# Optimization experiments

Hardware: AMD Instinct MI355X
Metric: run time of the kernel (lower is better)

The kernel has to match this reference:

```python
import jax, jax.numpy as jnp
import numpy as np

DIM = 64
N = 10000
E = 40000


def setup_inputs() -> dict:
    key = jax.random.key(0)
    ks = jax.random.split(key, 16)
    def rn(k, shape, s):
        return jax.random.normal(k, shape, dtype=jnp.float32) * s
    inp = {}
    inp["x"] = jax.random.normal(ks[0], (N, 3), dtype=jnp.float32)
    inp["edge_attr"] = jax.random.uniform(ks[1], (E, 7), dtype=jnp.float32)
    inp["edge_index"] = jax.random.randint(ks[2], (2, E), 0, N)
    inp["batch"] = jnp.zeros((N,), dtype=jnp.int32)
    # lin0: Linear(3, dim)
    inp["lin0_w"] = rn(ks[3], (DIM, 3), 0.3)
    inp["lin0_b"] = jnp.zeros((DIM,), jnp.float32)
    # edge MLP: Linear(7, dim) -> ReLU -> Linear(dim, dim*dim)
    inp["em1_w"] = rn(ks[4], (DIM, 7), 0.3)
    inp["em1_b"] = jnp.zeros((DIM,), jnp.float32)
    inp["em2_w"] = rn(ks[5], (DIM * DIM, DIM), 0.05)
    inp["em2_b"] = jnp.zeros((DIM * DIM,), jnp.float32)
    # NNConv root weight [in, out] and bias
    inp["root_w"] = rn(ks[6], (DIM, DIM), 0.1)
    inp["conv_b"] = jnp.zeros((DIM,), jnp.float32)
    # GRU(dim, dim), gate order r, z, n
    inp["gru_wih"] = rn(ks[7], (3 * DIM, DIM), 0.1)
    inp["gru_whh"] = rn(ks[8], (3 * DIM, DIM), 0.1)
    inp["gru_bih"] = jnp.zeros((3 * DIM,), jnp.float32)
    inp["gru_bhh"] = jnp.zeros((3 * DIM,), jnp.float32)
    # Set2Set LSTM(2*dim, dim), gate order i, f, g, o
    inp["lstm_wih"] = rn(ks[9], (4 * DIM, 2 * DIM), 0.1)
    inp["lstm_whh"] = rn(ks[10], (4 * DIM, DIM), 0.1)
    inp["lstm_bih"] = jnp.zeros((4 * DIM,), jnp.float32)
    inp["lstm_bhh"] = jnp.zeros((4 * DIM,), jnp.float32)
    inp["lin1_w"] = rn(ks[11], (DIM, 2 * DIM), 0.1)
    inp["lin1_b"] = jnp.zeros((DIM,), jnp.float32)
    inp["lin3_w"] = rn(ks[12], (1, DIM), 0.1)
    inp["lin3_b"] = jnp.zeros((1,), jnp.float32)
    return inp


def _forward(x, edge_attr, lin0_w, lin0_b, em1_w, em1_b, em2_w, em2_b,
             root_w, conv_b, gru_wih, gru_whh, gru_bih, gru_bhh,
             lstm_wih, lstm_whh, lstm_bih, lstm_bhh,
             lin1_w, lin1_b, lin3_w, lin3_b, edge_index, batch):
    n = x.shape[0]
    dim = lin0_w.shape[0]
    src, dst = edge_index[0], edge_index[1]

    out = jax.nn.relu(x @ lin0_w.T + lin0_b)  # [N, dim]
    h = out                                   # GRU hidden state

    # Edge-conditioned weights depend only on edge_attr -> compute once.
    we = jax.nn.relu(edge_attr @ em1_w.T + em1_b) @ em2_w.T + em2_b
    we = we.reshape(-1, dim, dim)             # [E, dim, dim]

    deg = jax.ops.segment_sum(jnp.ones_like(src, dtype=x.dtype), dst, num_segments=n)
    inv_deg = jnp.where(deg > 0, 1.0 / jnp.maximum(deg, 1.0), 0.0)[:, None]

    for _ in range(6):
        # NNConv: per-edge matmul, scatter-mean, plus root transform
        msg = jnp.einsum('ei,eio->eo', out[src], we)            # [E, dim]
        agg = jax.ops.segment_sum(msg, dst, num_segments=n) * inv_deg
        m = jax.nn.relu(out @ root_w + agg + conv_b)            # [N, dim]
        # single-step GRU over nodes (seq_len=1, batch=N)
        gi = m @ gru_wih.T + gru_bih
        gh = h @ gru_whh.T + gru_bhh
        ir, iz, inew = jnp.split(gi, 3, axis=-1)
        hr, hz, hnew = jnp.split(gh, 3, axis=-1)
        r = jax.nn.sigmoid(ir + hr)
        z = jax.nn.sigmoid(iz + hz)
        ncand = jnp.tanh(inew + r * hnew)
        h = (1.0 - z) * ncand + z * h
        out = h

    # Set2Set pooling; single graph (batch is all zeros, pool.view(1,-1))
    q_star = jnp.zeros((1, 2 * dim), x.dtype)
    hl = jnp.zeros((1, dim), x.dtype)
    cl = jnp.zeros((1, dim), x.dtype)
    for _ in range(6):
        g = q_star @ lstm_wih.T + lstm_bih + hl @ lstm_whh.T + lstm_bhh
        gi_, gf_, gg_, go_ = jnp.split(g, 4, axis=-1)
        cl = jax.nn.sigmoid(gf_) * cl + jax.nn.sigmoid(gi_) * jnp.tanh(gg_)
        hl = jax.nn.sigmoid(go_) * jnp.tanh(cl)
        q = hl                                                  # [1, dim]
        e = jnp.einsum('nd,d->n', out, q[0])                    # attention logits
        a = jax.nn.softmax(e)                                   # softmax over the single graph
        r = jnp.einsum('n,nd->d', a, out)[None, :]              # readout [1, dim]
        q_star = jnp.concatenate([q, r], axis=-1)               # [1, 2*dim]

    pool = q_star.reshape(1, -1)
    hid = jax.nn.relu(pool @ lin1_w.T + lin1_b)
    return hid @ lin3_w.T + lin3_b                              # [1, 1]


def reference(x, edge_attr, edge_index, batch, lin0_w, lin0_b, em1_w, em1_b,
              em2_w, em2_b, root_w, conv_b, gru_wih, gru_whh, gru_bih, gru_bhh,
              lstm_wih, lstm_whh, lstm_bih, lstm_bhh, lin1_w, lin1_b, lin3_w, lin3_b):
    return _forward(x, edge_attr, lin0_w, lin0_b, em1_w, em1_b, em2_w, em2_b,
                    root_w, conv_b, gru_wih, gru_whh, gru_bih, gru_bhh,
                    lstm_wih, lstm_whh, lstm_bih, lstm_bhh,
                    lin1_w, lin1_b, lin3_w, lin3_b, edge_index, batch)
```

## Files before the change

### kernel.cpp

```cpp
#include <hip/hip_runtime.h>
#include <math.h>

#define NNODES 10000
#define NEDGES 40000
#define DIM 64
#define MC 4160
#define WS 200
#define AST2 72

typedef short bf16x8 __attribute__((ext_vector_type(8)));
typedef float floatx4 __attribute__((ext_vector_type(4)));

__device__ __forceinline__ float sigmoidf_(float x) { return 1.0f / (1.0f + expf(-x)); }

__device__ __forceinline__ unsigned short f2bf(float x) {
    unsigned int u = __float_as_uint(x);
    u += 0x7fffu + ((u >> 16) & 1u);
    return (unsigned short)(u >> 16);
}
__device__ __forceinline__ float bf2f(unsigned short h) {
    return __uint_as_float(((unsigned int)h) << 16);
}
__device__ __forceinline__ void write_split(unsigned short* __restrict__ p, int d, float v) {
    unsigned short hi = f2bf(v);
    unsigned short lo = f2bf(v - bf2f(hi));
    p[d] = hi;
    p[64 + d] = hi;
    p[128 + d] = lo;
}

__global__ __launch_bounds__(256) void k_node_init(const float* __restrict__ x,
                                                   const float* __restrict__ w,
                                                   const float* __restrict__ b,
                                                   float* __restrict__ out,
                                                   unsigned short* __restrict__ Abf) {
    int idx = blockIdx.x * 256 + threadIdx.x;
    if (idx >= NNODES * 64) return;
    int n = idx >> 6, d = idx & 63;
    float a = b[d];
    a += x[n * 3 + 0] * w[d * 3 + 0];
    a += x[n * 3 + 1] * w[d * 3 + 1];
    a += x[n * 3 + 2] * w[d * 3 + 2];
    float v = fmaxf(a, 0.0f);
    out[idx] = v;
    write_split(Abf + (size_t)n * 192, d, v);
}

__global__ __launch_bounds__(256) void k_h1(const float* __restrict__ ea,
                                            const float* __restrict__ w,
                                            const float* __restrict__ b,
                                            const int* __restrict__ sortpos,
                                            float* __restrict__ h1s) {
    int idx = blockIdx.x * 256 + threadIdx.x;
    if (idx >= NEDGES * 64) return;
    int e = idx >> 6, d = idx & 63;
    float a = b[d];
#pragma unroll
    for (int j = 0; j < 7; ++j) a += ea[e * 7 + j] * w[d * 7 + j];
    h1s[(size_t)sortpos[e] * 64 + d] = fmaxf(a, 0.0f);
}

__global__ __launch_bounds__(256) void k_w2bt(const float* __restrict__ em2_w,
                                              const float* __restrict__ em2_b,
                                              unsigned short* __restrict__ Bbf) {
    int idx = blockIdx.x * 256 + threadIdx.x;
    if (idx >= 64 * MC) return;
    int c = idx >> 6, i = idx & 63;
    float v;
    if (c < 4096) {
        v = em2_w[((size_t)(i * 64 + (c >> 6))) * 64 + (c & 63)];
    } else {
        v = em2_b[i * 64 + (c - 4096)];
    }
    unsigned short hi = f2bf(v);
    unsigned short lo = f2bf(v - bf2f(hi));
    unsigned short* row = Bbf + (size_t)c * 192;
    row[i] = hi;
    row[64 + i] = lo;
    row[128 + i] = hi;
}

__global__ __launch_bounds__(256) void k_wb(const float* __restrict__ root_w,
                                            const float* __restrict__ wih,
                                            const float* __restrict__ whh,
                                            unsigned short* __restrict__ Wcat) {
    int idx = blockIdx.x * 256 + threadIdx.x;
    if (idx >= 448 * 64) return;
    int r = idx >> 6, i = idx & 63;
    float v;
    if (r < 64) v = root_w[i * 64 + r];
    else if (r < 256) v = wih[(r - 64) * 64 + i];
    else v = whh[(r - 256) * 64 + i];
    unsigned short hi = f2bf(v);
    unsigned short lo = f2bf(v - bf2f(hi));
    unsigned short* row = Wcat + (size_t)r * 192;
    row[i] = hi;
    row[64 + i] = lo;
    row[128 + i] = hi;
}

__global__ __launch_bounds__(256) void k_lstmT2(const float* __restrict__ wih,
                                                const float* __restrict__ whh,
                                                float* __restrict__ wcT,
                                                float* __restrict__ wrT) {
    int idx = blockIdx.x * 256 + threadIdx.x;
    if (idx < 64 * 256) {
        int k = idx >> 8, t = idx & 255;
        wcT[idx] = wih[t * 128 + k] + whh[t * 64 + k];
    } else if (idx < 2 * 64 * 256) {
        int i2 = idx - 64 * 256;
        int k = i2 >> 8, t = i2 & 255;
        wrT[i2] = wih[t * 128 + 64 + k];
    }
}

__global__ __launch_bounds__(256) void k_hist(const int* __restrict__ ei,
                                              int* __restrict__ counts,
                                              float* __restrict__ deg) {
    int e = blockIdx.x * 256 + threadIdx.x;
    if (e < NEDGES) {
        atomicAdd(&counts[ei[e]], 1);
        atomicAdd(&deg[ei[NEDGES + e]], 1.0f);
    }
}

__global__ __launch_bounds__(256) void k_scan(const int* __restrict__ counts,
                                              int* __restrict__ row_start,
                                              int* __restrict__ cursor) {
    __shared__ int partial[256];
    const int tid = threadIdx.x;
    const int base = tid * 40;
    int local[40];
    int sum = 0;
#pragma unroll
    for (int i = 0; i < 40; ++i) {
        int idx = base + i;
        int v = (idx < NNODES) ? counts[idx] : 0;
        local[i] = sum;
        sum += v;
    }
    partial[tid] = sum;
    __syncthreads();
    for (int off = 1; off < 256; off <<= 1) {
        int t = (tid >= off) ? partial[tid - off] : 0;
        __syncthreads();
        partial[tid] += t;
        __syncthreads();
    }
    const int prev = (tid > 0) ? partial[tid - 1] : 0;
#pragma unroll
    for (int i = 0; i < 40; ++i) {
        int idx = base + i;
        if (idx < NNODES) {
            int rs = prev + local[i];
            row_start[idx] = rs;
            cursor[idx] = rs;
        }
    }
    if (tid == 255) row_start[NNODES] = partial[255];
}

__global__ __launch_bounds__(256) void k_scatter(const int* __restrict__ ei,
                                                 int* __restrict__ cursor,
                                                 int* __restrict__ sortpos,
                                                 int* __restrict__ dst_s) {
    int e = blockIdx.x * 256 + threadIdx.x;
    if (e < NEDGES) {
        int s = ei[e];
        int pos = atomicAdd(&cursor[s], 1);
        sortpos[e] = pos;
        dst_s[pos] = ei[NEDGES + e];
    }
}

__global__ __launch_bounds__(256) void k_invdeg(const float* __restrict__ deg, float* __restrict__ inv) {
    int n = blockIdx.x * 256 + threadIdx.x;
    if (n < NNODES) {
        float dg = deg[n];
        inv[n] = dg > 0.0f ? 1.0f / dg : 0.0f;
    }
}

__global__ __launch_bounds__(256) void k_gemmM(const unsigned short* __restrict__ Abf,
                                               const unsigned short* __restrict__ Bbf,
                                               unsigned short* __restrict__ Mb) {
    __shared__ __align__(16) unsigned short As[64 * AST2];
    __shared__ __align__(16) unsigned short Bs[64 * AST2];
    __shared__ __align__(16) float Cs[64 * 68];
    const int tid = threadIdx.x;
    const int col0 = blockIdx.x * 64;
    const int wave = tid >> 6, lane = tid & 63;
    const int mi = lane & 15, q = lane >> 4;
#pragma unroll
    for (int j = 0; j < 2; ++j) {
        int idx = tid + 256 * j;
        int r = idx >> 3, c8 = (idx & 7) * 8;
        *reinterpret_cast<uint4*>(&Bs[r * AST2 + c8]) =
            *reinterpret_cast<const uint4*>(&Bbf[(size_t)(col0 + r) * 192 + c8]);
    }
    for (int rt = 0; rt < 4; ++rt) {
        const int row0 = (blockIdx.y * 4 + rt) * 64;
#pragma unroll
        for (int j = 0; j < 2; ++j) {
            int idx = tid + 256 * j;
            int r = idx >> 3, c8 = (idx & 7) * 8;
            int ra = row0 + r;
            if (ra >= NNODES) ra = NNODES - 1;
            *reinterpret_cast<uint4*>(&As[r * AST2 + c8]) =
                *reinterpret_cast<const uint4*>(&Abf[(size_t)ra * 192 + c8]);
        }
        __syncthreads();
        floatx4 acc[4];
#pragma unroll
        for (int nt = 0; nt < 4; ++nt)
#pragma unroll
            for (int r = 0; r < 4; ++r) acc[nt][r] = 0.0f;
        const unsigned short* arow = &As[(wave * 16 + mi) * AST2 + q * 8];
#pragma unroll
        for (int ks = 0; ks < 2; ++ks) {
            bf16x8 a = *reinterpret_cast<const bf16x8*>(arow + ks * 32);
#pragma unroll
            for (int nt = 0; nt < 4; ++nt) {
                bf16x8 b = *reinterpret_cast<const bf16x8*>(&Bs[(nt * 16 + mi) * AST2 + ks * 32 + q * 8]);
                acc[nt] = __builtin_amdgcn_mfma_f32_16x16x32_bf16(a, b, acc[nt], 0, 0, 0);
            }
        }
        const int rl = wave * 16 + q * 4;
#pragma unroll
        for (int nt = 0; nt < 4; ++nt)
#pragma unroll
            for (int r = 0; r < 4; ++r)
                Cs[(rl + r) * 68 + nt * 16 + mi] = acc[nt][r];
        __syncthreads();
#pragma unroll
        for (int j = 0; j < 2; ++j) {
            int idx = tid + 256 * j;
            int r = idx >> 3, c8 = (idx & 7) * 8;
            int row = row0 + r;
            if (row < NNODES) {
                const float* src = &Cs[r * 68 + c8];
                unsigned int p0 = (unsigned int)f2bf(src[0]) | ((unsigned int)f2bf(src[1]) << 16);
                unsigned int p1 = (unsigned int)f2bf(src[2]) | ((unsigned int)f2bf(src[3]) << 16);
                unsigned int p2 = (unsigned int)f2bf(src[4]) | ((unsigned int)f2bf(src[5]) << 16);
                unsigned int p3 = (unsigned int)f2bf(src[6]) | ((unsigned int)f2bf(src[7]) << 16);
                *reinterpret_cast<uint4*>(&Mb[(size_t)row * MC + col0 + c8]) =
                    make_uint4(p0, p1, p2, p3);
            }
        }
        __syncthreads();
    }
}

__global__ __launch_bounds__(256) void k_msg(const unsigned short* __restrict__ Mb,
                                             const float* __restrict__ h1s,
                                             const int* __restrict__ row_start,
                                             const int* __restrict__ dst_s,
                                             float* __restrict__ agg) {
    const int w = threadIdx.x >> 6;
    const int o = threadIdx.x & 63;
    const int s = blockIdx.x * 4 + w;
    const int e0 = row_start[s], e1 = row_start[s + 1];
    if (e0 == e1) return;
    const unsigned short* mrow = Mb + (size_t)s * MC + o * 64;
    uint4 m[8];
#pragma unroll
    for (int j = 0; j < 8; ++j)
        m[j] = *reinterpret_cast<const uint4*>(mrow + j * 8);
    const float bias = bf2f(Mb[(size_t)s * MC + 4096 + o]);
    for (int e = e0; e < e1; ++e) {
        const float4* hv = reinterpret_cast<const float4*>(h1s + (size_t)e * 64);
        float acc = bias;
#pragma unroll
        for (int j = 0; j < 8; ++j) {
            float4 ha = hv[2 * j];
            float4 hb = hv[2 * j + 1];
            unsigned int u;
            u = m[j].x;
            acc += ha.x * __uint_as_float(u << 16) + ha.y * __uint_as_float(u & 0xffff0000u);
            u = m[j].y;
            acc += ha.z * __uint_as_float(u << 16) + ha.w * __uint_as_float(u & 0xffff0000u);
            u = m[j].z;
            acc += hb.x * __uint_as_float(u << 16) + hb.y * __uint_as_float(u & 0xffff0000u);
            u = m[j].w;
            acc += hb.z * __uint_as_float(u << 16) + hb.w * __uint_as_float(u & 0xffff0000u);
        }
        atomicAdd(&agg[(size_t)dst_s[e] * 64 + o], acc);
    }
}

__global__ __launch_bounds__(256) void k_node(float* __restrict__ agg,
                                              const float* __restrict__ invdeg,
                                              const unsigned short* __restrict__ Wcat,
                                              const float* __restrict__ conv_b,
                                              const float* __restrict__ bih,
                                              const float* __restrict__ bhh,
                                              float* __restrict__ out,
                                              unsigned short* __restrict__ Abf) {
    __shared__ unsigned short As[64 * WS];
    __shared__ unsigned short Ms[64 * WS];
    __shared__ unsigned short Bs[192 * WS];
    __shared__ float ho[64 * 68];
    const int tid = threadIdx.x;
    const int row0 = blockIdx.x * 64;
#pragma unroll
    for (int j = 0; j < 6; ++j) {
        int idx = tid + 256 * j;
        int r = idx / 24, jj = idx % 24;
        int ra = row0 + r; if (ra >= NNODES) ra = NNODES - 1;
        *reinterpret_cast<uint4*>(&As[r * WS + jj * 8]) =
            *reinterpret_cast<const uint4*>(&Abf[(size_t)ra * 192 + jj * 8]);
    }
#pragma unroll
    for (int j = 0; j < 4; ++j) {
        int idx = tid + 256 * j;
        int r = idx >> 4, c4 = (idx & 15) * 4;
        int ra = row0 + r; if (ra >= NNODES) ra = NNODES - 1;
        *reinterpret_cast<float4*>(&ho[r * 68 + c4]) =
            *reinterpret_cast<const float4*>(&out[(size_t)ra * 64 + c4]);
    }
#pragma unroll
    for (int j = 0; j < 18; ++j) {
        int idx = tid + 256 * j;
        int r = idx / 24, jj = idx % 24;
        *reinterpret_cast<uint4*>(&Bs[r * WS + jj * 8]) =
            *reinterpret_cast<const uint4*>(&Wcat[(size_t)(256 + r) * 192 + jj * 8]);
    }
    __syncthreads();
    const int wave = tid >> 6, lane = tid & 63;
    const int mi = lane & 15, q = lane >> 4;
    const int d = wave * 16 + mi;
    floatx4 gh[4][3];
#pragma unroll
    for (int rt = 0; rt < 4; ++rt)
#pragma unroll
        for (int g = 0; g < 3; ++g)
#pragma unroll
            for (int r = 0; r < 4; ++r) gh[rt][g][r] = 0.0f;
#pragma unroll
    for (int ks = 0; ks < 6; ++ks) {
        bf16x8 b[3];
#pragma unroll
        for (int g = 0; g < 3; ++g)
            b[g] = *reinterpret_cast<const bf16x8*>(&Bs[(g * 64 + d) * WS + ks * 32 + q * 8]);
#pragma unroll
        for (int rt = 0; rt < 4; ++rt) {
            bf16x8 a = *reinterpret_cast<const bf16x8*>(&As[(rt * 16 + mi) * WS + ks * 32 + q * 8]);
#pragma unroll
            for (int g = 0; g < 3; ++g)
                gh[rt][g] = __builtin_amdgcn_mfma_f32_16x16x32_bf16(a, b[g], gh[rt][g], 0, 0, 0);
        }
    }
    __syncthreads();
#pragma unroll
    for (int j = 0; j < 6; ++j) {
        int idx = tid + 256 * j;
        int r = idx / 24, jj = idx % 24;
        *reinterpret_cast<uint4*>(&Bs[r * WS + jj * 8]) =
            *reinterpret_cast<const uint4*>(&Wcat[(size_t)r * 192 + jj * 8]);
    }
    __syncthreads();
    {
        floatx4 cm[4];
#pragma unroll
        for (int rt = 0; rt < 4; ++rt)
#pragma unroll
            for (int r = 0; r < 4; ++r) cm[rt][r] = 0.0f;
#pragma unroll
        for (int ks = 0; ks < 6; ++ks) {
            bf16x8 b = *reinterpret_cast<const bf16x8*>(&Bs[d * WS + ks * 32 + q * 8]);
#pragma unroll
            for (int rt = 0; rt < 4; ++rt) {
                bf16x8 a = *reinterpret_cast<const bf16x8*>(&As[(rt * 16 + mi) * WS + ks * 32 + q * 8]);
                cm[rt] = __builtin_amdgcn_mfma_f32_16x16x32_bf16(a, b, cm[rt], 0, 0, 0);
            }
        }
        const float cb = conv_b[d];
#pragma unroll
        for (int rt = 0; rt < 4; ++rt) {
#pragma unroll
            for (int r = 0; r < 4; ++r) {
                int row = rt * 16 + q * 4 + r;
                int ra = row0 + row; int rc = (ra < NNODES) ? ra : NNODES - 1;
                float v = cm[rt][r] + agg[(size_t)rc * 64 + d] * invdeg[rc] + cb;
                if (ra < NNODES) agg[(size_t)ra * 64 + d] = 0.0f;
                v = fmaxf(v, 0.0f);
                unsigned short hi = f2bf(v);
                unsigned short lo = f2bf(v - bf2f(hi));
                Ms[row * WS + d] = hi;
                Ms[row * WS + 64 + d] = hi;
                Ms[row * WS + 128 + d] = lo;
            }
        }
    }
    __syncthreads();
#pragma unroll
    for (int j = 0; j < 18; ++j) {
        int idx = tid + 256 * j;
        int r = idx / 24, jj = idx % 24;
        *reinterpret_cast<uint4*>(&Bs[r * WS + jj * 8]) =
            *reinterpret_cast<const uint4*>(&Wcat[(size_t)(64 + r) * 192 + jj * 8]);
    }
    __syncthreads();
    floatx4 gi[4][3];
#pragma unroll
    for (int rt = 0; rt < 4; ++rt)
#pragma unroll
        for (int g = 0; g < 3; ++g)
#pragma unroll
            for (int r = 0; r < 4; ++r) gi[rt][g][r] = 0.0f;
#pragma unroll
    for (int ks = 0; ks < 6; ++ks) {
        bf16x8 b[3];
#pragma unroll
        for (int g = 0; g < 3; ++g)
            b[g] = *reinterpret_cast<const bf16x8*>(&Bs[(g * 64 + d) * WS + ks * 32 + q * 8]);
#pragma unroll
        for (int rt = 0; rt < 4; ++rt) {
            bf16x8 a = *reinterpret_cast<const bf16x8*>(&Ms[(rt * 16 + mi) * WS + ks * 32 + q * 8]);
#pragma unroll
            for (int g = 0; g < 3; ++g)
                gi[rt][g] = __builtin_amdgcn_mfma_f32_16x16x32_bf16(a, b[g], gi[rt][g], 0, 0, 0);
        }
    }
    const float bi_r = bih[d], bi_z = bih[64 + d], bi_n = bih[128 + d];
    const float bh_r = bhh[d], bh_z = bhh[64 + d], bh_n = bhh[128 + d];
#pragma unroll
    for (int rt = 0; rt < 4; ++rt) {
#pragma unroll
        for (int r = 0; r < 4; ++r) {
            int row = rt * 16 + q * 4 + r;
            int ra = row0 + row;
            float rr = sigmoidf_(gi[rt][0][r] + bi_r + gh[rt][0][r] + bh_r);
            float zz = sigmoidf_(gi[rt][1][r] + bi_z + gh[rt][1][r] + bh_z);
            float nc = tanhf(gi[rt][2][r] + bi_n + rr * (gh[rt][2][r] + bh_n));
            float hn = (1.0f - zz) * nc + zz * ho[row * 68 + d];
            if (ra < NNODES) {
                out[(size_t)ra * 64 + d] = hn;
                write_split(Abf + (size_t)ra * 192, d, hn);
            }
        }
    }
}

__global__ __launch_bounds__(256) void k_step(const float* __restrict__ out,
                                              const float* __restrict__ wcT,
                                              const float* __restrict__ wrT,
                                              const float* __restrict__ bih,
                                              const float* __restrict__ bhh,
                                              float* __restrict__ hc,
                                              float* rs,
                                              int it) {
    __shared__ float outs[256 * 65];
    __shared__ float hl_s[64];
    __shared__ float qr[64];
    __shared__ float gsh[256];
    __shared__ float wsh[256];
    __shared__ float red[256];
    const int tid = threadIdx.x;
    const int n0 = blockIdx.x * 256;
#pragma unroll
    for (int j = 0; j < 16; ++j) {
        int idx = tid + 256 * j;
        int r = idx >> 4, c4 = (idx & 15) * 4;
        int n = n0 + r;
        float4 v = make_float4(0.0f, 0.0f, 0.0f, 0.0f);
        if (n < NNODES) v = *reinterpret_cast<const float4*>(&out[(size_t)n * 64 + c4]);
        outs[r * 65 + c4 + 0] = v.x;
        outs[r * 65 + c4 + 1] = v.y;
        outs[r * 65 + c4 + 2] = v.z;
        outs[r * 65 + c4 + 3] = v.w;
    }
    if (tid < 64) {
        hl_s[tid] = hc[it * 128 + tid];
        qr[tid] = (it > 0) ? rs[it * 68 + tid] / rs[it * 68 + 64] : 0.0f;
    }
    __syncthreads();
    float g0 = 0.0f, g1 = 0.0f, g2 = 0.0f, g3 = 0.0f;
#pragma unroll 4
    for (int k = 0; k < 64; k += 4) {
        g0 += hl_s[k + 0] * wcT[(k + 0) * 256 + tid] + qr[k + 0] * wrT[(k + 0) * 256 + tid];
        g1 += hl_s[k + 1] * wcT[(k + 1) * 256 + tid] + qr[k + 1] * wrT[(k + 1) * 256 + tid];
        g2 += hl_s[k + 2] * wcT[(k + 2) * 256 + tid] + qr[k + 2] * wrT[(k + 2) * 256 + tid];
        g3 += hl_s[k + 3] * wcT[(k + 3) * 256 + tid] + qr[k + 3] * wrT[(k + 3) * 256 + tid];
    }
    gsh[tid] = bih[tid] + bhh[tid] + ((g0 + g1) + (g2 + g3));
    __syncthreads();
    if (tid < 64) {
        float ig = sigmoidf_(gsh[tid]);
        float fg = sigmoidf_(gsh[64 + tid]);
        float gg = tanhf(gsh[128 + tid]);
        float og = sigmoidf_(gsh[192 + tid]);
        float c = fg * hc[it * 128 + 64 + tid] + ig * gg;
        float h = og * tanhf(c);
        hl_s[tid] = h;
        hc[(it + 1) * 128 + tid] = h;
        hc[(it + 1) * 128 + 64 + tid] = c;
    }
    __syncthreads();
    float w = 0.0f;
    if (n0 + tid < NNODES) {
        const float* row = &outs[tid * 65];
        float e0 = 0.0f, e1 = 0.0f, e2 = 0.0f, e3 = 0.0f;
#pragma unroll 8
        for (int k = 0; k < 64; k += 4) {
            e0 += row[k + 0] * hl_s[k + 0];
            e1 += row[k + 1] * hl_s[k + 1];
            e2 += row[k + 2] * hl_s[k + 2];
            e3 += row[k + 3] * hl_s[k + 3];
        }
        w = expf((e0 + e1) + (e2 + e3));
    }
    wsh[tid] = w;
    red[tid] = w;
    __syncthreads();
    for (int s = 128; s > 0; s >>= 1) {
        if (tid < s) red[tid] += red[tid + s];
        __syncthreads();
    }
    if (tid == 0) atomicAdd(&rs[(it + 1) * 68 + 64], red[0]);
    const int grp = tid >> 6, d = tid & 63;
    float a0 = 0.0f, a1 = 0.0f;
#pragma unroll 8
    for (int j = 0; j < 64; j += 2) {
        a0 += wsh[grp * 64 + j] * outs[(grp * 64 + j) * 65 + d];
        a1 += wsh[grp * 64 + j + 1] * outs[(grp * 64 + j + 1) * 65 + d];
    }
    atomicAdd(&rs[(it + 1) * 68 + d], a0 + a1);
}

__global__ __launch_bounds__(128) void k_out(const float* __restrict__ hc,
                                             const float* __restrict__ rs,
                                             const float* __restrict__ lin1_w,
                                             const float* __restrict__ lin1_b,
                                             const float* __restrict__ lin3_w,
                                             const float* __restrict__ lin3_b,
                                             float* __restrict__ dout) {
    __shared__ float qs[128];
    __shared__ float hs[64];
    int tid = threadIdx.x;
    qs[tid] = (tid < 64) ? hc[6 * 128 + tid] : rs[6 * 68 + (tid - 64)] / rs[6 * 68 + 64];
    __syncthreads();
    if (tid < 64) {
        float a = lin1_b[tid];
        for (int k = 0; k < 128; ++k) a += qs[k] * lin1_w[tid * 128 + k];
        hs[tid] = fmaxf(a, 0.0f);
    }
    __syncthreads();
    if (tid == 0) {
        float a = lin3_b[0];
        for (int k = 0; k < 64; ++k) a += hs[k] * lin3_w[k];
        dout[0] = a;
    }
}

extern "C" void kernel_launch(void* const* d_in, const int* in_sizes, int n_in,
                              void* d_out, int out_size, void* d_ws, size_t ws_size,
                              hipStream_t stream) {
    const float* x         = (const float*)d_in[0];
    const float* edge_attr = (const float*)d_in[1];
    const int*   ei        = (const int*)d_in[2];
    const float* lin0_w    = (const float*)d_in[4];
    const float* lin0_b    = (const float*)d_in[5];
    const float* em1_w     = (const float*)d_in[6];
    const float* em1_b     = (const float*)d_in[7];
    const float* em2_w     = (const float*)d_in[8];
    const float* em2_b     = (const float*)d_in[9];
    const float* root_w    = (const float*)d_in[10];
    const float* conv_b    = (const float*)d_in[11];
    const float* gru_wih   = (const float*)d_in[12];
    const float* gru_whh   = (const float*)d_in[13];
    const float* gru_bih   = (const float*)d_in[14];
    const float* gru_bhh   = (const float*)d_in[15];
    const float* lstm_wih  = (const float*)d_in[16];
    const float* lstm_whh  = (const float*)d_in[17];
    const float* lstm_bih  = (const float*)d_in[18];
    const float* lstm_bhh  = (const float*)d_in[19];
    const float* lin1_w    = (const float*)d_in[20];
    const float* lin1_b    = (const float*)d_in[21];
    const float* lin3_w    = (const float*)d_in[22];
    const float* lin3_b    = (const float*)d_in[23];

    float* ws = (float*)d_ws;
    size_t off = 0;
    unsigned short* Mb   = (unsigned short*)(ws + off); off += (size_t)NNODES * MC / 2;
    unsigned short* Abf  = (unsigned short*)(ws + off); off += (size_t)NNODES * 192 / 2;
    unsigned short* Bbf  = (unsigned short*)(ws + off); off += (size_t)MC * 192 / 2;
    unsigned short* Wcat = (unsigned short*)(ws + off); off += (size_t)448 * 192 / 2;
    float* h1s   = ws + off; off += (size_t)NEDGES * 64;
    float* outb  = ws + off; off += (size_t)NNODES * 64;
    float* agg   = ws + off; off += (size_t)NNODES * 64;
    float* deg   = ws + off; off += NNODES;
    int*   counts    = (int*)(ws + off); off += NNODES;
    int*   cursor    = (int*)(ws + off); off += NNODES;
    int*   row_start = (int*)(ws + off); off += NNODES + 4;
    int*   sortpos   = (int*)(ws + off); off += NEDGES;
    int*   dst_s     = (int*)(ws + off); off += NEDGES;
    float* invd  = ws + off; off += NNODES;
    float* wcT   = ws + off; off += 64 * 256;
    float* wrT   = ws + off; off += 64 * 256;
    float* rs    = ws + off; off += 7 * 68;
    float* hc    = ws + off; off += 7 * 128;

    k_node_init<<<2500, 256, 0, stream>>>(x, lin0_w, lin0_b, outb, Abf);
    k_w2bt<<<(64 * MC + 255) / 256, 256, 0, stream>>>(em2_w, em2_b, Bbf);
    k_wb<<<(448 * 64 + 255) / 256, 256, 0, stream>>>(root_w, gru_wih, gru_whh, Wcat);
    k_lstmT2<<<128, 256, 0, stream>>>(lstm_wih, lstm_whh, wcT, wrT);
    hipMemsetAsync(deg, 0, 3 * NNODES * sizeof(float), stream);
    hipMemsetAsync(agg, 0, (size_t)NNODES * 64 * sizeof(float), stream);
    hipMemsetAsync(rs, 0, (7 * 68 + 7 * 128) * sizeof(float), stream);
    k_hist<<<(NEDGES + 255) / 256, 256, 0, stream>>>(ei, counts, deg);
    k_scan<<<1, 256, 0, stream>>>(counts, row_start, cursor);
    k_scatter<<<(NEDGES + 255) / 256, 256, 0, stream>>>(ei, cursor, sortpos, dst_s);
    k_invdeg<<<(NNODES + 255) / 256, 256, 0, stream>>>(deg, invd);
    k_h1<<<10000, 256, 0, stream>>>(edge_attr, em1_w, em1_b, sortpos, h1s);

    for (int t = 0; t < 6; ++t) {
        k_gemmM<<<dim3(65, 40), 256, 0, stream>>>(Abf, Bbf, Mb);
        k_msg<<<2500, 256, 0, stream>>>(Mb, h1s, row_start, dst_s, agg);
        k_node<<<157, 256, 0, stream>>>(agg, invd, Wcat, conv_b, gru_bih, gru_bhh,
                                        outb, Abf);
    }

    for (int it = 0; it < 6; ++it)
        k_step<<<40, 256, 0, stream>>>(outb, wcT, wrT, lstm_bih, lstm_bhh, hc, rs, it);
    k_out<<<1, 128, 0, stream>>>(hc, rs, lin1_w, lin1_b, lin3_w, lin3_b, (float*)d_out);
}
```

Before: 687.8 us.

## Fuse per-node message-weight GEMM with edge message aggregation via LDS

Merges the GEMM that produced the per-node bf16 message matrix (10000 x 4160) with the edge message kernel. Each 512-thread block computes the matrices for 14 source nodes into shared memory and immediately uses them to process those nodes' outgoing edges. This removes the large global write and re-read of the intermediate matrix in every iteration. In exchange it uses about 131 KB of LDS per block, which limits occupancy, and B fragments are read straight from global memory by each block without LDS staging.

New measurement: 810.9 us. 1.18x slower.

```diff
diff --git a/kernel.cpp b/kernel.cpp
--- a/kernel.cpp
+++ b/kernel.cpp
@@ -4,9 +4,10 @@
 #define NNODES 10000
 #define NEDGES 40000
 #define DIM 64
-#define MC 4160
 #define WS 200
-#define AST2 72
+#define MROWS 14
+#define MGS 72
+#define MRS 4680
 
 typedef short bf16x8 __attribute__((ext_vector_type(8)));
 typedef float floatx4 __attribute__((ext_vector_type(4)));
@@ -64,7 +65,7 @@
                                               const float* __restrict__ em2_b,
                                               unsigned short* __restrict__ Bbf) {
     int idx = blockIdx.x * 256 + threadIdx.x;
-    if (idx >= 64 * MC) return;
+    if (idx >= 64 * 4160) return;
     int c = idx >> 6, i = idx & 63;
     float v;
     if (c < 4096) {
@@ -181,110 +182,111 @@
     }
 }
 
-__global__ __launch_bounds__(256) void k_gemmM(const unsigned short* __restrict__ Abf,
+__global__ __launch_bounds__(512) void k_fused(const unsigned short* __restrict__ Abf,
                                                const unsigned short* __restrict__ Bbf,
-                                               unsigned short* __restrict__ Mb) {
-    __shared__ __align__(16) unsigned short As[64 * AST2];
-    __shared__ __align__(16) unsigned short Bs[64 * AST2];
-    __shared__ __align__(16) float Cs[64 * 68];
+                                               const float* __restrict__ h1s,
+                                               const int* __restrict__ row_start,
+                                               const int* __restrict__ dst_s,
+                                               float* __restrict__ agg) {
+    __shared__ __align__(16) unsigned short Mush[MROWS * MRS];
     const int tid = threadIdx.x;
-    const int col0 = blockIdx.x * 64;
-    const int wave = tid >> 6, lane = tid & 63;
+    const int w = tid >> 6, lane = tid & 63;
     const int mi = lane & 15, q = lane >> 4;
-#pragma unroll
-    for (int j = 0; j < 2; ++j) {
-        int idx = tid + 256 * j;
-        int r = idx >> 3, c8 = (idx & 7) * 8;
-        *reinterpret_cast<uint4*>(&Bs[r * AST2 + c8]) =
-            *reinterpret_cast<const uint4*>(&Bbf[(size_t)(col0 + r) * 192 + c8]);
-    }
-    for (int rt = 0; rt < 4; ++rt) {
-        const int row0 = (blockIdx.y * 4 + rt) * 64;
-#pragma unroll
-        for (int j = 0; j < 2; ++j) {
-            int idx = tid + 256 * j;
-            int r = idx >> 3, c8 = (idx & 7) * 8;
-            int ra = row0 + r;
-            if (ra >= NNODES) ra = NNODES - 1;
-            *reinterpret_cast<uint4*>(&As[r * AST2 + c8]) =
-                *reinterpret_cast<const uint4*>(&Abf[(size_t)ra * 192 + c8]);
-        }
-        __syncthreads();
-        floatx4 acc[4];
-#pragma unroll
-        for (int nt = 0; nt < 4; ++nt)
-#pragma unroll
-            for (int r = 0; r < 4; ++r) acc[nt][r] = 0.0f;
-        const unsigned short* arow = &As[(wave * 16 + mi) * AST2 + q * 8];
-#pragma unroll
-        for (int ks = 0; ks < 2; ++ks) {
-            bf16x8 a = *reinterpret_cast<const bf16x8*>(arow + ks * 32);
+    const int s0 = blockIdx.x * MROWS;
+    int ar = s0 + mi; if (ar >= NNODES) ar = NNODES - 1;
+    const bf16x8 a0 = *reinterpret_cast<const bf16x8*>(&Abf[(size_t)ar * 192 + q * 8]);
+    const bf16x8 a1 = *reinterpret_cast<const bf16x8*>(&Abf[(size_t)ar * 192 + 32 + q * 8]);
+    for (int c = w; c < 65; c += 16) {
+        const int c2 = c + 8;
+        bf16x8 bA[8], bB[8];
+#pragma unroll
+        for (int nt = 0; nt < 4; ++nt) {
+            const size_t rb = (size_t)(c * 64 + nt * 16 + mi) * 192;
+            bA[nt]     = *reinterpret_cast<const bf16x8*>(&Bbf[rb + q * 8]);
+            bA[4 + nt] = *reinterpret_cast<const bf16x8*>(&Bbf[rb + 32 + q * 8]);
+        }
+        if (c2 < 65) {
 #pragma unroll
             for (int nt = 0; nt < 4; ++nt) {
-                bf16x8 b = *reinterpret_cast<const bf16x8*>(&Bs[(nt * 16 + mi) * AST2 + ks * 32 + q * 8]);
-                acc[nt] = __builtin_amdgcn_mfma_f32_16x16x32_bf16(a, b, acc[nt], 0, 0, 0);
+                const size_t rb = (size_t)(c2 * 64 + nt * 16 + mi) * 192;
+                bB[nt]     = *reinterpret_cast<const bf16x8*>(&Bbf[rb + q * 8]);
+                bB[4 + nt] = *reinterpret_cast<const bf16x8*>(&Bbf[rb + 32 + q * 8]);
             }
         }
-        const int rl = wave * 16 + q * 4;
-#pragma unroll
-        for (int nt = 0; nt < 4; ++nt)
-#pragma unroll
-            for (int r = 0; r < 4; ++r)
-                Cs[(rl + r) * 68 + nt * 16 + mi] = acc[nt][r];
-        __syncthreads();
-#pragma unroll
-        for (int j = 0; j < 2; ++j) {
-            int idx = tid + 256 * j;
-            int r = idx >> 3, c8 = (idx & 7) * 8;
-            int row = row0 + r;
-            if (row < NNODES) {
-                const float* src = &Cs[r * 68 + c8];
-                unsigned int p0 = (unsigned int)f2bf(src[0]) | ((unsigned int)f2bf(src[1]) << 16);
-                unsigned int p1 = (unsigned int)f2bf(src[2]) | ((unsigned int)f2bf(src[3]) << 16);
-                unsigned int p2 = (unsigned int)f2bf(src[4]) | ((unsigned int)f2bf(src[5]) << 16);
-                unsigned int p3 = (unsigned int)f2bf(src[6]) | ((unsigned int)f2bf(src[7]) << 16);
-                *reinterpret_cast<uint4*>(&Mb[(size_t)row * MC + col0 + c8]) =
-                    make_uint4(p0, p1, p2, p3);
+        {
+            floatx4 acc[4];
+#pragma unroll
+            for (int nt = 0; nt < 4; ++nt)
+#pragma unroll
+                for (int r = 0; r < 4; ++r) acc[nt][r] = 0.0f;
+#pragma unroll
+            for (int nt = 0; nt < 4; ++nt) {
+                acc[nt] = __builtin_amdgcn_mfma_f32_16x16x32_bf16(a0, bA[nt], acc[nt], 0, 0, 0);
+                acc[nt] = __builtin_amdgcn_mfma_f32_16x16x32_bf16(a1, bA[4 + nt], acc[nt], 0, 0, 0);
             }
-        }
-        __syncthreads();
-    }
-}
-
-__global__ __launch_bounds__(256) void k_msg(const unsigned short* __restrict__ Mb,
-                                             const float* __restrict__ h1s,
-                                             const int* __restrict__ row_start,
-                                             const int* __restrict__ dst_s,
-                                             float* __restrict__ agg) {
-    const int w = threadIdx.x >> 6;
-    const int o = threadIdx.x & 63;
-    const int s = blockIdx.x * 4 + w;
-    const int e0 = row_start[s], e1 = row_start[s + 1];
-    if (e0 == e1) return;
-    const unsigned short* mrow = Mb + (size_t)s * MC + o * 64;
-    uint4 m[8];
-#pragma unroll
-    for (int j = 0; j < 8; ++j)
-        m[j] = *reinterpret_cast<const uint4*>(mrow + j * 8);
-    const float bias = bf2f(Mb[(size_t)s * MC + 4096 + o]);
-    for (int e = e0; e < e1; ++e) {
-        const float4* hv = reinterpret_cast<const float4*>(h1s + (size_t)e * 64);
-        float acc = bias;
-#pragma unroll
-        for (int j = 0; j < 8; ++j) {
-            float4 ha = hv[2 * j];
-            float4 hb = hv[2 * j + 1];
-            unsigned int u;
-            u = m[j].x;
-            acc += ha.x * __uint_as_float(u << 16) + ha.y * __uint_as_float(u & 0xffff0000u);
-            u = m[j].y;
-            acc += ha.z * __uint_as_float(u << 16) + ha.w * __uint_as_float(u & 0xffff0000u);
-            u = m[j].z;
-            acc += hb.x * __uint_as_float(u << 16) + hb.y * __uint_as_float(u & 0xffff0000u);
-            u = m[j].w;
-            acc += hb.z * __uint_as_float(u << 16) + hb.w * __uint_as_float(u & 0xffff0000u);
-        }
-        atomicAdd(&agg[(size_t)dst_s[e] * 64 + o], acc);
+#pragma unroll
+            for (int nt = 0; nt < 4; ++nt)
+#pragma unroll
+                for (int r = 0; r < 4; ++r) {
+                    int rr = q * 4 + r;
+                    if (rr < MROWS)
+                        Mush[rr * MRS + c * MGS + nt * 16 + mi] = f2bf(acc[nt][r]);
+                }
+        }
+        if (c2 < 65) {
+            floatx4 acc[4];
+#pragma unroll
+            for (int nt = 0; nt < 4; ++nt)
+#pragma unroll
+                for (int r = 0; r < 4; ++r) acc[nt][r] = 0.0f;
+#pragma unroll
+            for (int nt = 0; nt < 4; ++nt) {
+                acc[nt] = __builtin_amdgcn_mfma_f32_16x16x32_bf16(a0, bB[nt], acc[nt], 0, 0, 0);
+                acc[nt] = __builtin_amdgcn_mfma_f32_16x16x32_bf16(a1, bB[4 + nt], acc[nt], 0, 0, 0);
+            }
+#pragma unroll
+            for (int nt = 0; nt < 4; ++nt)
+#pragma unroll
+                for (int r = 0; r < 4; ++r) {
+                    int rr = q * 4 + r;
+                    if (rr < MROWS)
+                        Mush[rr * MRS + c2 * MGS + nt * 16 + mi] = f2bf(acc[nt][r]);
+                }
+        }
+    }
+    __syncthreads();
+#pragma unroll
+    for (int t = 0; t < 2; ++t) {
+        const int sl = w * 2 + t;
+        if (sl >= MROWS) continue;
+        const int s = s0 + sl;
+        if (s >= NNODES) continue;
+        const int e0 = row_start[s], e1 = row_start[s + 1];
+        if (e0 == e1) continue;
+        uint4 m[8];
+#pragma unroll
+        for (int j = 0; j < 8; ++j)
+            m[j] = *reinterpret_cast<const uint4*>(&Mush[sl * MRS + lane * MGS + j * 8]);
+        const float bias = bf2f(Mush[sl * MRS + 64 * MGS + lane]);
+        for (int e = e0; e < e1; ++e) {
+            const float4* hv = reinterpret_cast<const float4*>(h1s + (size_t)e * 64);
+            float acc = bias;
+#pragma unroll
+            for (int j = 0; j < 8; ++j) {
+                float4 ha = hv[2 * j];
+                float4 hb = hv[2 * j + 1];
+                unsigned int u;
+                u = m[j].x;
+                acc += ha.x * __uint_as_float(u << 16) + ha.y * __uint_as_float(u & 0xffff0000u);
+                u = m[j].y;
+                acc += ha.z * __uint_as_float(u << 16) + ha.w * __uint_as_float(u & 0xffff0000u);
+                u = m[j].z;
+                acc += hb.x * __uint_as_float(u << 16) + hb.y * __uint_as_float(u & 0xffff0000u);
+                u = m[j].w;
+                acc += hb.z * __uint_as_float(u << 16) + hb.w * __uint_as_float(u & 0xffff0000u);
+            }
+            atomicAdd(&agg[(size_t)dst_s[e] * 64 + lane], acc);
+        }
     }
 }
 
@@ -582,9 +584,8 @@
 
     float* ws = (float*)d_ws;
     size_t off = 0;
-    unsigned short* Mb   = (unsigned short*)(ws + off); off += (size_t)NNODES * MC / 2;
     unsigned short* Abf  = (unsigned short*)(ws + off); off += (size_t)NNODES * 192 / 2;
-    unsigned short* Bbf  = (unsigned short*)(ws + off); off += (size_t)MC * 192 / 2;
+    unsigned short* Bbf  = (unsigned short*)(ws + off); off += (size_t)4160 * 192 / 2;
     unsigned short* Wcat = (unsigned short*)(ws + off); off += (size_t)448 * 192 / 2;
     float* h1s   = ws + off; off += (size_t)NEDGES * 64;
     float* outb  = ws + off; off += (size_t)NNODES * 64;
@@ -602,7 +603,7 @@
     float* hc    = ws + off; off += 7 * 128;
 
     k_node_init<<<2500, 256, 0, stream>>>(x, lin0_w, lin0_b, outb, Abf);
-    k_w2bt<<<(64 * MC + 255) / 256, 256, 0, stream>>>(em2_w, em2_b, Bbf);
+    k_w2bt<<<(64 * 4160 + 255) / 256, 256, 0, stream>>>(em2_w, em2_b, Bbf);
     k_wb<<<(448 * 64 + 255) / 256, 256, 0, stream>>>(root_w, gru_wih, gru_whh, Wcat);
     k_lstmT2<<<128, 256, 0, stream>>>(lstm_wih, lstm_whh, wcT, wrT);
     hipMemsetAsync(deg, 0, 3 * NNODES * sizeof(float), stream);
@@ -614,9 +615,9 @@
     k_invdeg<<<(NNODES + 255) / 256, 256, 0, stream>>>(deg, invd);
     k_h1<<<10000, 256, 0, stream>>>(edge_attr, em1_w, em1_b, sortpos, h1s);
 
+    const int nfb = (NNODES + MROWS - 1) / MROWS;
     for (int t = 0; t < 6; ++t) {
-        k_gemmM<<<dim3(65, 40), 256, 0, stream>>>(Abf, Bbf, Mb);
-        k_msg<<<2500, 256, 0, stream>>>(Mb, h1s, row_start, dst_s, agg);
+        k_fused<<<nfb, 512, 0, stream>>>(Abf, Bbf, h1s, row_start, dst_s, agg);
         k_node<<<157, 256, 0, stream>>>(agg, invd, Wcat, conv_b, gru_bih, gru_bhh,
                                         outb, Abf);
     }
```

## Halve k_node row tile and read GRU weights directly from global

Applied to the files above, without the earlier changes.

The node-update kernel now handles 32 rows per block instead of 64, doubling the grid to 313 blocks so more of the GPU's compute units get work. It also drops the shared-memory staging of the weight matrices (Bs) and the syncthreads around it, loading the B fragments straight from global memory or L2. This cuts shared memory use and barriers, but each weight fragment is now fetched once per block from global rather than reused from LDS, which doubles total weight traffic.

Measured after the change: 691.4 us. About the same (+0.5%).

```diff
diff --git a/kernel.cpp b/kernel.cpp
--- a/kernel.cpp
+++ b/kernel.cpp
@@ -296,14 +296,13 @@
                                               const float* __restrict__ bhh,
                                               float* __restrict__ out,
                                               unsigned short* __restrict__ Abf) {
-    __shared__ unsigned short As[64 * WS];
-    __shared__ unsigned short Ms[64 * WS];
-    __shared__ unsigned short Bs[192 * WS];
-    __shared__ float ho[64 * 68];
+    __shared__ unsigned short As[32 * WS];
+    __shared__ unsigned short Ms[32 * WS];
+    __shared__ float ho[32 * 68];
     const int tid = threadIdx.x;
-    const int row0 = blockIdx.x * 64;
-#pragma unroll
-    for (int j = 0; j < 6; ++j) {
+    const int row0 = blockIdx.x * 32;
+#pragma unroll
+    for (int j = 0; j < 3; ++j) {
         int idx = tid + 256 * j;
         int r = idx / 24, jj = idx % 24;
         int ra = row0 + r; if (ra >= NNODES) ra = NNODES - 1;
@@ -311,27 +310,20 @@
             *reinterpret_cast<const uint4*>(&Abf[(size_t)ra * 192 + jj * 8]);
     }
 #pragma unroll
-    for (int j = 0; j < 4; ++j) {
+    for (int j = 0; j < 2; ++j) {
         int idx = tid + 256 * j;
         int r = idx >> 4, c4 = (idx & 15) * 4;
         int ra = row0 + r; if (ra >= NNODES) ra = NNODES - 1;
         *reinterpret_cast<float4*>(&ho[r * 68 + c4]) =
             *reinterpret_cast<const float4*>(&out[(size_t)ra * 64 + c4]);
     }
-#pragma unroll
-    for (int j = 0; j < 18; ++j) {
-        int idx = tid + 256 * j;
-        int r = idx / 24, jj = idx % 24;
-        *reinterpret_cast<uint4*>(&Bs[r * WS + jj * 8]) =
-            *reinterpret_cast<const uint4*>(&Wcat[(size_t)(256 + r) * 192 + jj * 8]);
-    }
     __syncthreads();
     const int wave = tid >> 6, lane = tid & 63;
     const int mi = lane & 15, q = lane >> 4;
     const int d = wave * 16 + mi;
-    floatx4 gh[4][3];
-#pragma unroll
-    for (int rt = 0; rt < 4; ++rt)
+    floatx4 gh[2][3];
+#pragma unroll
+    for (int rt = 0; rt < 2; ++rt)
 #pragma unroll
         for (int g = 0; g < 3; ++g)
 #pragma unroll
@@ -341,42 +333,33 @@
         bf16x8 b[3];
 #pragma unroll
         for (int g = 0; g < 3; ++g)
-            b[g] = *reinterpret_cast<const bf16x8*>(&Bs[(g * 64 + d) * WS + ks * 32 + q * 8]);
-#pragma unroll
-        for (int rt = 0; rt < 4; ++rt) {
+            b[g] = *reinterpret_cast<const bf16x8*>(&Wcat[(size_t)(256 + g * 64 + d) * 192 + ks * 32 + q * 8]);
+#pragma unroll
+        for (int rt = 0; rt < 2; ++rt) {
             bf16x8 a = *reinterpret_cast<const bf16x8*>(&As[(rt * 16 + mi) * WS + ks * 32 + q * 8]);
 #pragma unroll
             for (int g = 0; g < 3; ++g)
                 gh[rt][g] = __builtin_amdgcn_mfma_f32_16x16x32_bf16(a, b[g], gh[rt][g], 0, 0, 0);
         }
     }
-    __syncthreads();
-#pragma unroll
-    for (int j = 0; j < 6; ++j) {
-        int idx = tid + 256 * j;
-        int r = idx / 24, jj = idx % 24;
-        *reinterpret_cast<uint4*>(&Bs[r * WS + jj * 8]) =
-            *reinterpret_cast<const uint4*>(&Wcat[(size_t)r * 192 + jj * 8]);
-    }
-    __syncthreads();
     {
-        floatx4 cm[4];
-#pragma unroll
-        for (int rt = 0; rt < 4; ++rt)
+        floatx4 cm[2];
+#pragma unroll
+        for (int rt = 0; rt < 2; ++rt)
 #pragma unroll
             for (int r = 0; r < 4; ++r) cm[rt][r] = 0.0f;
 #pragma unroll
         for (int ks = 0; ks < 6; ++ks) {
-            bf16x8 b = *reinterpret_cast<const bf16x8*>(&Bs[d * WS + ks * 32 + q * 8]);
-#pragma unroll
-            for (int rt = 0; rt < 4; ++rt) {
+            bf16x8 b = *reinterpret_cast<const bf16x8*>(&Wcat[(size_t)d * 192 + ks * 32 + q * 8]);
+#pragma unroll
+            for (int rt = 0; rt < 2; ++rt) {
                 bf16x8 a = *reinterpret_cast<const bf16x8*>(&As[(rt * 16 + mi) * WS + ks * 32 + q * 8]);
                 cm[rt] = __builtin_amdgcn_mfma_f32_16x16x32_bf16(a, b, cm[rt], 0, 0, 0);
             }
         }
         const float cb = conv_b[d];
 #pragma unroll
-        for (int rt = 0; rt < 4; ++rt) {
+        for (int rt = 0; rt < 2; ++rt) {
 #pragma unroll
             for (int r = 0; r < 4; ++r) {
                 int row = rt * 16 + q * 4 + r;
@@ -393,17 +376,9 @@
         }
     }
     __syncthreads();
-#pragma unroll
-    for (int j = 0; j < 18; ++j) {
-        int idx = tid + 256 * j;
-        int r = idx / 24, jj = idx % 24;
-        *reinterpret_cast<uint4*>(&Bs[r * WS + jj * 8]) =
-            *reinterpret_cast<const uint4*>(&Wcat[(size_t)(64 + r) * 192 + jj * 8]);
-    }
-    __syncthreads();
-    floatx4 gi[4][3];
-#pragma unroll
-    for (int rt = 0; rt < 4; ++rt)
+    floatx4 gi[2][3];
+#pragma unroll
+    for (int rt = 0; rt < 2; ++rt)
 #pragma unroll
         for (int g = 0; g < 3; ++g)
 #pragma unroll
@@ -413,9 +388,9 @@
         bf16x8 b[3];
 #pragma unroll
         for (int g = 0; g < 3; ++g)
-            b[g] = *reinterpret_cast<const bf16x8*>(&Bs[(g * 64 + d) * WS + ks * 32 + q * 8]);
-#pragma unroll
-        for (int rt = 0; rt < 4; ++rt) {
+            b[g] = *reinterpret_cast<const bf16x8*>(&Wcat[(size_t)(64 + g * 64 + d) * 192 + ks * 32 + q * 8]);
+#pragma unroll
+        for (int rt = 0; rt < 2; ++rt) {
             bf16x8 a = *reinterpret_cast<const bf16x8*>(&Ms[(rt * 16 + mi) * WS + ks * 32 + q * 8]);
 #pragma unroll
             for (int g = 0; g < 3; ++g)
@@ -425,7 +400,7 @@
     const float bi_r = bih[d], bi_z = bih[64 + d], bi_n = bih[128 + d];
     const float bh_r = bhh[d], bh_z = bhh[64 + d], bh_n = bhh[128 + d];
 #pragma unroll
-    for (int rt = 0; rt < 4; ++rt) {
+    for (int rt = 0; rt < 2; ++rt) {
 #pragma unroll
         for (int r = 0; r < 4; ++r) {
             int row = rt * 16 + q * 4 + r;
@@ -617,7 +592,7 @@
     for (int t = 0; t < 6; ++t) {
         k_gemmM<<<dim3(65, 40), 256, 0, stream>>>(Abf, Bbf, Mb);
         k_msg<<<2500, 256, 0, stream>>>(Mb, h1s, row_start, dst_s, agg);
-        k_node<<<157, 256, 0, stream>>>(agg, invd, Wcat, conv_b, gru_bih, gru_bhh,
+        k_node<<<313, 256, 0, stream>>>(agg, invd, Wcat, conv_b, gru_bih, gru_bhh,
                                         outb, Abf);
     }
 
```
